# Performance work log

Hardware: AMD Instinct MI355X
Metric: run time of the kernel (lower is better)

## Reference

```python
import jax, jax.numpy as jnp
import numpy as np

THRESHOLD = 0.5
NEG_POS_RATIO = 3
ALPHA = 1.0


def xywh2xyxy(b):
    return jnp.concatenate([b[:, :2], b[:, :2] + b[:, 2:]], axis=1)


def cxcy2xyxy(b):
    return jnp.concatenate([b[:, :2] - b[:, 2:] / 2, b[:, :2] + b[:, 2:] / 2], axis=1)


def xyxy2cxcy(b):
    return jnp.concatenate([(b[:, :2] + b[:, 2:]) / 2, b[:, 2:] - b[:, :2]], axis=1)


def jaccard(a, b):
    # a: [n,4], b: [m,4] in xyxy -> IoU [n,m]
    lt = jnp.maximum(a[:, None, :2], b[None, :, :2])
    rb = jnp.minimum(a[:, None, 2:], b[None, :, 2:])
    wh = jnp.clip(rb - lt, 0.0)
    inter = wh[..., 0] * wh[..., 1]
    area_a = (a[:, 2] - a[:, 0]) * (a[:, 3] - a[:, 1])
    area_b = (b[:, 2] - b[:, 0]) * (b[:, 3] - b[:, 1])
    return inter / (area_a[:, None] + area_b[None, :] - inter)


def encode(cxcy, priors_cxcy):
    # cxcy_to_gcxgcy: offsets scaled by /10 variance, log sizes scaled by *5
    return jnp.concatenate([
        (cxcy[:, :2] - priors_cxcy[:, :2]) / (priors_cxcy[:, 2:] / 10.0),
        jnp.log(jnp.abs(cxcy[:, 2:] / priors_cxcy[:, 2:])) * 5.0,
    ], axis=1)


def _match_one(boxes_xywh, labels_i, priors_xy, priors_cxcy):
    n_obj = boxes_xywh.shape[0]
    b_xyxy = xywh2xyxy(boxes_xywh)                      # [n_obj,4]
    ov = jaccard(b_xyxy, priors_xy)                     # [n_obj, P]
    ovl_p = ov.max(axis=0)                              # [P]
    obj_p = ov.argmax(axis=0)                           # [P]
    prior_for_obj = ov.argmax(axis=1)                   # [n_obj]
    # force each object to own its best prior
    obj_p = obj_p.at[prior_for_obj].set(jnp.arange(n_obj))
    ovl_p = ovl_p.at[prior_for_obj].set(1.0)
    lab = labels_i[obj_p]                               # [P]
    lab = jnp.where(ovl_p < THRESHOLD, 0, lab)
    ignore = (ovl_p > 0.4) & (ovl_p < 0.5)
    true_locs = encode(xyxy2cxcy(b_xyxy[obj_p]), priors_cxcy)  # [P,4]
    return lab, ignore, true_locs


def _smooth_l1(x):
    ax = jnp.abs(x)
    return jnp.where(ax < 1.0, 0.5 * ax * ax, ax - 0.5)


def multibox_loss(predicted_locs, predicted_scores, boxes, labels, priors_cxcy):
    priors_xy = cxcy2xyxy(priors_cxcy)
    true_classes, ignored, true_locs = jax.vmap(
        _match_one, in_axes=(0, 0, None, None))(boxes, labels, priors_xy, priors_cxcy)
    pos = (true_classes > 0) & (~ignored)               # [B,P]
    n_pos = pos.sum(axis=1)                             # [B]
    n_pos_total = n_pos.sum()

    # localization loss: SmoothL1 mean over positive-prior elements
    loc_elem = _smooth_l1(predicted_locs - true_locs)   # [B,P,4]
    loc_loss = (loc_elem * pos[..., None]).sum() / (n_pos_total.astype(jnp.float32) * 4.0)

    # per-prior cross entropy
    logp = jax.nn.log_softmax(predicted_scores, axis=-1)           # [B,P,C]
    ce = -jnp.take_along_axis(logp, true_classes[..., None], axis=-1)[..., 0]  # [B,P]

    conf_pos_sum = (ce * pos).sum()
    ce_neg = jnp.where(pos | ignored, 0.0, ce)
    ce_neg_sorted = -jnp.sort(-ce_neg, axis=1)          # descending per row
    ranks = jnp.arange(ce.shape[1])[None, :]
    hard = ranks < (NEG_POS_RATIO * n_pos)[:, None]
    conf_loss = (jnp.where(hard, ce_neg_sorted, 0.0).sum() + conf_pos_sum) / n_pos_total.astype(jnp.float32)

    total = conf_loss + ALPHA * loc_loss
    return total, conf_loss, loc_loss


def setup_inputs() -> dict:
    key = jax.random.key(0)
    k1, k2, k3, k4, k5, k6 = jax.random.split(key, 6)
    B, P, C, NOBJ = 64, 8732, 91, 16
    predicted_locs = jax.random.normal(k1, (B, P, 4), dtype=jnp.float32)
    predicted_scores = jax.random.normal(k2, (B, P, C), dtype=jnp.float32)
    xy = jax.random.uniform(k3, (B, NOBJ, 2)) * 0.6
    wh = jax.random.uniform(k4, (B, NOBJ, 2)) * 0.35 + 0.05
    boxes = jnp.concatenate([xy, wh], axis=-1).astype(jnp.float32)  # xywh
    labels = jax.random.randint(k5, (B, NOBJ), 1, C)
    pxy = jax.random.uniform(k6, (P, 2))
    pwh = jax.random.uniform(jax.random.fold_in(k6, 1), (P, 2)) * 0.45 + 0.05
    priors_cxcy = jnp.concatenate([pxy, pwh], axis=-1).astype(jnp.float32)
    return {"predicted_locs": predicted_locs, "predicted_scores": predicted_scores,
            "boxes": boxes, "labels": labels, "priors_cxcy": priors_cxcy}


def reference(predicted_locs, predicted_scores, boxes, labels, priors_cxcy):
    return multibox_loss(predicted_locs, predicted_scores, boxes, labels, priors_cxcy)
```

## Files before the change

kernel.cpp:

```cpp
#include <hip/hip_runtime.h>
#include <math.h>

#define TPB 256
#define MTPB 512
#define CE_BLOCKS 2048

__device__ __forceinline__ float sl1(float x) {
    float a = fabsf(x);
    return a < 1.f ? 0.5f * a * a : a - 0.5f;
}

template<int NOBJ>
__global__ __launch_bounds__(MTPB)
void k_match(const float* __restrict__ boxes, const int* __restrict__ labels,
             const float* __restrict__ priors, const float* __restrict__ plocs,
             int P, unsigned* __restrict__ meta, int* __restrict__ n_pos,
             float* __restrict__ loc_sum, unsigned* __restrict__ ticket)
{
    const int b = blockIdx.x;
    const int tid = threadIdx.x;
    const int NW = MTPB / 64;

    if (b == 0 && tid == 0) *ticket = 0u;

    extern __shared__ char smem[];
    float* ovl_s = (float*)smem;
    unsigned char* obj_s = (unsigned char*)(smem + (size_t)P * 4);
    char* base2 = smem + (size_t)P * 4 + (size_t)((P + 15) & ~15);
    float* sbox2 = (float*)base2;
    int*   s_lab = (int*)(base2 + 4 * NOBJ * 4);
    float* redv  = (float*)(base2 + 5 * NOBJ * 4);
    int*   redp  = (int*)(base2 + (5 + NW) * NOBJ * 4);
    int*   pf    = (int*)(base2 + (5 + 2 * NW) * NOBJ * 4);
    int*   s_cnt = pf + NOBJ;
    float* s_lsum = (float*)(s_cnt + 1);

    float bx1[NOBJ], by1[NOBJ], bx2[NOBJ], by2[NOBJ], bar[NOBJ];
#pragma unroll
    for (int o = 0; o < NOBJ; o++) {
        const float4 bx = ((const float4*)boxes)[(size_t)b * NOBJ + o];
        bx1[o] = bx.x; by1[o] = bx.y;
        bx2[o] = bx.x + bx.z; by2[o] = bx.y + bx.w;
        bar[o] = (bx2[o] - bx1[o]) * (by2[o] - by1[o]);
    }
    if (tid < NOBJ) {
        sbox2[0 * NOBJ + tid] = (bx1[tid] + bx2[tid]) * 0.5f;
        sbox2[1 * NOBJ + tid] = (by1[tid] + by2[tid]) * 0.5f;
        sbox2[2 * NOBJ + tid] = bx2[tid] - bx1[tid];
        sbox2[3 * NOBJ + tid] = by2[tid] - by1[tid];
        s_lab[tid] = labels[b * NOBJ + tid];
        if (tid == 0) { *s_cnt = 0; *s_lsum = 0.f; }
    }

    float bestv[NOBJ];
    int bestp[NOBJ];
#pragma unroll
    for (int o = 0; o < NOBJ; o++) { bestv[o] = -1.f; bestp[o] = 0x7fffffff; }

    for (int p = tid; p < P; p += MTPB) {
        float4 pr = ((const float4*)priors)[p];
        float hx = pr.z * 0.5f, hy = pr.w * 0.5f;
        float px1 = pr.x - hx, py1 = pr.y - hy;
        float px2 = pr.x + hx, py2 = pr.y + hy;
        float parea = (px2 - px1) * (py2 - py1);
        float bv = -1.f; int bo = 0;
#pragma unroll
        for (int o = 0; o < NOBJ; o++) {
            float ltx = fmaxf(bx1[o], px1);
            float lty = fmaxf(by1[o], py1);
            float rbx = fminf(bx2[o], px2);
            float rby = fminf(by2[o], py2);
            float w = rbx - ltx; w = w > 0.f ? w : 0.f;
            float h = rby - lty; h = h > 0.f ? h : 0.f;
            float inter = w * h;
            float iou = __fdividef(inter, bar[o] + parea - inter);
            if (iou > bv) { bv = iou; bo = o; }
            if (iou > bestv[o]) { bestv[o] = iou; bestp[o] = p; }
        }
        ovl_s[p] = bv;
        obj_s[p] = (unsigned char)bo;
    }

#pragma unroll
    for (int o = 0; o < NOBJ; o++) {
        float v = bestv[o]; int pp = bestp[o];
#pragma unroll
        for (int d = 1; d < 64; d <<= 1) {
            float v2 = __shfl_xor(v, d);
            int   q2 = __shfl_xor(pp, d);
            if (v2 > v || (v2 == v && q2 < pp)) { v = v2; pp = q2; }
        }
        if ((tid & 63) == 0) {
            redv[o * NW + (tid >> 6)] = v;
            redp[o * NW + (tid >> 6)] = pp;
        }
    }
    __syncthreads();

    if (tid < NOBJ) {
        float v = -2.f; int pp = 0x7fffffff;
        for (int w = 0; w < NW; w++) {
            float v2 = redv[tid * NW + w];
            int   q2 = redp[tid * NW + w];
            if (v2 > v || (v2 == v && q2 < pp)) { v = v2; pp = q2; }
        }
        pf[tid] = pp;
    }
    __syncthreads();

    if (tid == 0) {
        for (int i = 0; i < NOBJ; i++) {
            int pp = pf[i];
            obj_s[pp] = (unsigned char)i;
            ovl_s[pp] = 1.0f;
        }
    }
    __syncthreads();

    int cnt = 0;
    float lsum = 0.f;
    for (int p = tid; p < P; p += MTPB) {
        float ovl = ovl_s[p];
        int o = obj_s[p];
        int lab = s_lab[o];
        if (ovl < 0.5f) lab = 0;
        bool ign = (ovl > 0.4f) && (ovl < 0.5f);
        bool pos = (lab > 0) && !ign;
        meta[(size_t)b * P + p] = (unsigned)lab | (pos ? 256u : 0u) | (ign ? 512u : 0u);
        if (pos) {
            cnt++;
            float4 pr = ((const float4*)priors)[p];
            float cx = sbox2[0 * NOBJ + o], cy = sbox2[1 * NOBJ + o];
            float bw = sbox2[2 * NOBJ + o], bh = sbox2[3 * NOBJ + o];
            float g0 = (cx - pr.x) / (pr.z / 10.0f);
            float g1 = (cy - pr.y) / (pr.w / 10.0f);
            float g2 = __logf(fabsf(bw / pr.z)) * 5.0f;
            float g3 = __logf(fabsf(bh / pr.w)) * 5.0f;
            float4 pl = ((const float4*)plocs)[(size_t)b * P + p];
            lsum += sl1(pl.x - g0) + sl1(pl.y - g1) + sl1(pl.z - g2) + sl1(pl.w - g3);
        }
    }
#pragma unroll
    for (int d = 1; d < 64; d <<= 1) {
        lsum += __shfl_xor(lsum, d);
        cnt  += __shfl_xor(cnt, d);
    }
    if ((tid & 63) == 0) {
        atomicAdd(s_cnt, cnt);
        atomicAdd(s_lsum, lsum);
    }
    __syncthreads();
    if (tid == 0) {
        n_pos[b] = *s_cnt;
        loc_sum[b] = *s_lsum;
    }
}

__global__ __launch_bounds__(TPB)
void k_ce(const float* __restrict__ scores, const unsigned* __restrict__ meta,
          int BP, int C, float* __restrict__ ce_neg, float* __restrict__ pos_blk)
{
    const int tid = threadIdx.x;
    const int g = tid >> 4;
    const int wg = (tid >> 4) & 3;
    const int l = tid & 15;
    const int tiles = BP >> 4;

    float psum = 0.f;

    for (int t = blockIdx.x; t < tiles; t += gridDim.x) {
        const int row = (t << 4) + g;
        const unsigned mt = meta[row];
        const float* s = scores + (size_t)row * C;

        float v[6];
        float m = -INFINITY;
#pragma unroll
        for (int j = 0; j < 6; j++) {
            int idx = l + (j << 4);
            v[j] = (idx < C) ? s[idx] : -INFINITY;
            m = fmaxf(m, v[j]);
        }
#pragma unroll
        for (int d = 1; d < 16; d <<= 1) m = fmaxf(m, __shfl_xor(m, d));

        float se = 0.f;
#pragma unroll
        for (int j = 0; j < 6; j++) se += __expf(v[j] - m);
#pragma unroll
        for (int d = 1; d < 16; d <<= 1) se += __shfl_xor(se, d);

        const int lab = (int)(mt & 255u);
        float pick = v[0];
#pragma unroll
        for (int j = 1; j < 6; j++) pick = ((lab >> 4) == j) ? v[j] : pick;
        float sv = __shfl(pick, (wg << 4) | (lab & 15));

        if (l == 0) {
            float ce = __logf(se) + m - sv;
            bool pos = (mt >> 8) & 1u;
            bool ign = (mt >> 9) & 1u;
            ce_neg[row] = (pos || ign) ? 0.f : ce;
            if (pos) psum += ce;
        }
    }

#pragma unroll
    for (int d = 1; d < 64; d <<= 1) psum += __shfl_xor(psum, d);
    __shared__ float sp[4];
    if ((tid & 63) == 0) sp[tid >> 6] = psum;
    __syncthreads();
    if (tid == 0) pos_blk[blockIdx.x] = sp[0] + sp[1] + sp[2] + sp[3];
}

template<int ITEMS>
__global__ __launch_bounds__(MTPB)
void k_topk_final(const float* __restrict__ ce_neg, const int* __restrict__ n_pos,
                  const float* __restrict__ loc_sum, const float* __restrict__ pos_blk,
                  int nposblk, int P, int B,
                  float* __restrict__ hard, unsigned* __restrict__ ticket,
                  float* __restrict__ out)
{
    const int b = blockIdx.x;
    const int tid = threadIdx.x;
    const float* row = ce_neg + (size_t)b * P;
    __shared__ unsigned cnt[256];
    __shared__ float sm[256];
    __shared__ float s_sumhigh;
    __shared__ unsigned s_pref;
    __shared__ int s_krem;
    __shared__ bool s_last;

    int k = 3 * n_pos[b];
    if (k > P) k = P;

    float vals[ITEMS];
#pragma unroll
    for (int i = 0; i < ITEMS; i++) {
        int p = tid + i * MTPB;
        vals[i] = (p < P) ? row[p] : 0.f;
    }

    float hard_b = 0.f;
    if (k > 0) {
        if (tid == 0) { s_sumhigh = 0.f; s_pref = 0u; s_krem = k; }

        for (int shift = 24; shift >= 0; shift -= 8) {
            if (tid < 256) { cnt[tid] = 0u; sm[tid] = 0.f; }
            __syncthreads();

            if (shift == 24) {
#pragma unroll
                for (int i = 0; i < ITEMS; i++) {
                    int p = tid + i * MTPB;
                    float vv = vals[i];
                    unsigned bin = __float_as_uint(vv) >> 24;
                    bool done = (p >= P);
                    while (__any(!done)) {
                        unsigned long long act = __ballot(!done);
                        int leader = (int)__ffsll(act) - 1;
                        unsigned lb = (unsigned)__shfl((int)bin, leader);
                        bool mine = (!done) && (bin == lb);
                        float contrib = mine ? vv : 0.f;
#pragma unroll
                        for (int d = 1; d < 64; d <<= 1)
                            contrib += __shfl_xor(contrib, d);
                        unsigned long long grp = __ballot(mine);
                        if ((tid & 63) == leader) {
                            atomicAdd(&cnt[lb], (unsigned)__popcll(grp));
                            atomicAdd(&sm[lb], contrib);
                        }
                        done = done || mine;
                    }
                }
            } else {
                unsigned pref = s_pref;
                const int high = shift + 8;
#pragma unroll
                for (int i = 0; i < ITEMS; i++) {
                    int p = tid + i * MTPB;
                    float vv = vals[i];
                    unsigned u = __float_as_uint(vv);
                    if (p < P && ((u >> high) == (pref >> high))) {
                        unsigned bin = (u >> shift) & 255u;
                        atomicAdd(&cnt[bin], 1u);
                        atomicAdd(&sm[bin], vv);
                    }
                }
            }
            __syncthreads();
            if (tid == 0) {
                int krem = s_krem;
                float sh = s_sumhigh;
                unsigned p2 = s_pref;
                for (int bin = 255; bin >= 0; --bin) {
                    if ((int)cnt[bin] < krem) { krem -= (int)cnt[bin]; sh += sm[bin]; }
                    else { p2 |= ((unsigned)bin) << shift; break; }
                }
                s_krem = krem; s_sumhigh = sh; s_pref = p2;
            }
            __syncthreads();
        }
        if (tid == 0) {
            float t = __uint_as_float(s_pref);
            hard_b = s_sumhigh + (float)s_krem * t;
        }
    }

    if (tid == 0) {
        atomicExch(&hard[b], hard_b);
        __threadfence();
        unsigned old = atomicAdd(ticket, 1u);
        s_last = (old == (unsigned)(gridDim.x - 1));
    }
    __syncthreads();
    if (!s_last) return;

    __threadfence();
    float hd = (tid < B) ? atomicAdd(&hard[tid], 0.f) : 0.f;
    float lc = (tid < B) ? loc_sum[tid] : 0.f;
    int   np = (tid < B) ? n_pos[tid] : 0;
    float ps = 0.f;
    for (int i = tid; i < nposblk; i += MTPB) ps += pos_blk[i];

#pragma unroll
    for (int d = 1; d < 64; d <<= 1) {
        hd += __shfl_xor(hd, d);
        lc += __shfl_xor(lc, d);
        ps += __shfl_xor(ps, d);
        np += __shfl_xor(np, d);
    }
    if ((tid & 63) == 0) {
        int wv = tid >> 6;
        sm[wv] = hd; sm[8 + wv] = lc; sm[16 + wv] = ps;
        cnt[wv] = (unsigned)np;
    }
    __syncthreads();
    if (tid == 0) {
        float thd = 0.f, tlc = 0.f, tps = 0.f; unsigned tnp = 0u;
        for (int wv = 0; wv < MTPB / 64; wv++) {
            thd += sm[wv]; tlc += sm[8 + wv]; tps += sm[16 + wv]; tnp += cnt[wv];
        }
        float n = (float)tnp;
        float conf = (thd + tps) / n;
        float loc = tlc / (n * 4.0f);
        out[0] = conf + loc;
        out[1] = conf;
        out[2] = loc;
    }
}

extern "C" void kernel_launch(void* const* d_in, const int* in_sizes, int n_in,
                              void* d_out, int out_size, void* d_ws, size_t ws_size,
                              hipStream_t stream)
{
    const float* plocs  = (const float*)d_in[0];
    const float* scores = (const float*)d_in[1];
    const float* boxes  = (const float*)d_in[2];
    const int*   labels = (const int*)d_in[3];
    const float* priors = (const float*)d_in[4];

    const int P = in_sizes[4] / 4;
    const int B = in_sizes[0] / (P * 4);
    const int C = in_sizes[1] / (B * P);
    const int BP = B * P;

    char* ws = (char*)d_ws;
    float*    loc_sum = (float*)ws;
    int*      n_pos   = (int*)(ws + 1024);
    float*    hard    = (float*)(ws + 2048);
    unsigned* ticket  = (unsigned*)(ws + 3072);
    unsigned* meta    = (unsigned*)(ws + 4096);
    float*    ce_neg  = (float*)(ws + 4096 + (size_t)BP * 4);
    float*    pos_blk = (float*)(ws + 4096 + (size_t)BP * 8);

    size_t ldsA = (size_t)P * 4 + (size_t)((P + 15) & ~15) + 2048;
    k_match<16><<<B, MTPB, ldsA, stream>>>(boxes, labels, priors, plocs,
                                           P, meta, n_pos, loc_sum, ticket);

    k_ce<<<CE_BLOCKS, TPB, 0, stream>>>(scores, meta, BP, C, ce_neg, pos_blk);

    if (P <= MTPB * 18) {
        k_topk_final<18><<<B, MTPB, 0, stream>>>(ce_neg, n_pos, loc_sum, pos_blk,
                                                 CE_BLOCKS, P, B, hard, ticket,
                                                 (float*)d_out);
    } else {
        k_topk_final<36><<<B, MTPB, 0, stream>>>(ce_neg, n_pos, loc_sum, pos_blk,
                                                 CE_BLOCKS, P, B, hard, ticket,
                                                 (float*)d_out);
    }
}
```

Measured before the change: 162.7 us.

## Split prior matching into segmented kernels and add vectorized C=91 CE kernel

The single per-image matching kernel, which ran only B blocks, is split into an IoU kernel and a finalize kernel. Each runs B*4 blocks over segments of priors and exchanges per-prior overlap and object index through global memory. Per-segment best-prior reductions are merged in the finalize step, and positive counts and loc sums are kept per segment. A specialized cross-entropy kernel for 91 classes loads four rows per wave as coalesced float4 reads staged through LDS. The aim is more GPU occupancy for matching and better memory efficiency for the score read, at the cost of an extra launch and a global round-trip for the overlap data.

```diff
diff --git a/kernel.cpp b/kernel.cpp
--- a/kernel.cpp
+++ b/kernel.cpp
@@ -4,6 +4,7 @@
 #define TPB 256
 #define MTPB 512
 #define CE_BLOCKS 2048
+#define SEGS 4
 
 __device__ __forceinline__ float sl1(float x) {
     float a = fabsf(x);
@@ -12,28 +13,25 @@
 
 template<int NOBJ>
 __global__ __launch_bounds__(MTPB)
-void k_match(const float* __restrict__ boxes, const int* __restrict__ labels,
-             const float* __restrict__ priors, const float* __restrict__ plocs,
-             int P, unsigned* __restrict__ meta, int* __restrict__ n_pos,
-             float* __restrict__ loc_sum, unsigned* __restrict__ ticket)
+void k_match_iou(const float* __restrict__ boxes, const float* __restrict__ priors,
+                 int P, float* __restrict__ ovl_g, unsigned char* __restrict__ obj_g,
+                 float* __restrict__ segv, int* __restrict__ segp,
+                 unsigned* __restrict__ ticket)
 {
-    const int b = blockIdx.x;
+    const int bs = blockIdx.x;
+    const int b = bs >> 2;
+    const int s = bs & 3;
     const int tid = threadIdx.x;
     const int NW = MTPB / 64;
 
-    if (b == 0 && tid == 0) *ticket = 0u;
-
-    extern __shared__ char smem[];
-    float* ovl_s = (float*)smem;
-    unsigned char* obj_s = (unsigned char*)(smem + (size_t)P * 4);
-    char* base2 = smem + (size_t)P * 4 + (size_t)((P + 15) & ~15);
-    float* sbox2 = (float*)base2;
-    int*   s_lab = (int*)(base2 + 4 * NOBJ * 4);
-    float* redv  = (float*)(base2 + 5 * NOBJ * 4);
-    int*   redp  = (int*)(base2 + (5 + NW) * NOBJ * 4);
-    int*   pf    = (int*)(base2 + (5 + 2 * NW) * NOBJ * 4);
-    int*   s_cnt = pf + NOBJ;
-    float* s_lsum = (float*)(s_cnt + 1);
+    if (bs == 0 && tid == 0) *ticket = 0u;
+
+    __shared__ float redv[NOBJ * (MTPB / 64)];
+    __shared__ int   redp[NOBJ * (MTPB / 64)];
+
+    const int seglen = (P + SEGS - 1) / SEGS;
+    const int p0 = s * seglen;
+    const int p1 = min(p0 + seglen, P);
 
     float bx1[NOBJ], by1[NOBJ], bx2[NOBJ], by2[NOBJ], bar[NOBJ];
 #pragma unroll
@@ -43,21 +41,13 @@
         bx2[o] = bx.x + bx.z; by2[o] = bx.y + bx.w;
         bar[o] = (bx2[o] - bx1[o]) * (by2[o] - by1[o]);
     }
-    if (tid < NOBJ) {
-        sbox2[0 * NOBJ + tid] = (bx1[tid] + bx2[tid]) * 0.5f;
-        sbox2[1 * NOBJ + tid] = (by1[tid] + by2[tid]) * 0.5f;
-        sbox2[2 * NOBJ + tid] = bx2[tid] - bx1[tid];
-        sbox2[3 * NOBJ + tid] = by2[tid] - by1[tid];
-        s_lab[tid] = labels[b * NOBJ + tid];
-        if (tid == 0) { *s_cnt = 0; *s_lsum = 0.f; }
-    }
 
     float bestv[NOBJ];
     int bestp[NOBJ];
 #pragma unroll
     for (int o = 0; o < NOBJ; o++) { bestv[o] = -1.f; bestp[o] = 0x7fffffff; }
 
-    for (int p = tid; p < P; p += MTPB) {
+    for (int p = p0 + tid; p < p1; p += MTPB) {
         float4 pr = ((const float4*)priors)[p];
         float hx = pr.z * 0.5f, hy = pr.w * 0.5f;
         float px1 = pr.x - hx, py1 = pr.y - hy;
@@ -77,8 +67,8 @@
             if (iou > bv) { bv = iou; bo = o; }
             if (iou > bestv[o]) { bestv[o] = iou; bestp[o] = p; }
         }
-        ovl_s[p] = bv;
-        obj_s[p] = (unsigned char)bo;
+        ovl_g[(size_t)b * P + p] = bv;
+        obj_g[(size_t)b * P + p] = (unsigned char)bo;
     }
 
 #pragma unroll
@@ -104,24 +94,65 @@
             int   q2 = redp[tid * NW + w];
             if (v2 > v || (v2 == v && q2 < pp)) { v = v2; pp = q2; }
         }
+        segv[((size_t)b * NOBJ + tid) * SEGS + s] = v;
+        segp[((size_t)b * NOBJ + tid) * SEGS + s] = pp;
+    }
+}
+
+template<int NOBJ>
+__global__ __launch_bounds__(MTPB)
+void k_match_fin(const float* __restrict__ boxes, const int* __restrict__ labels,
+                 const float* __restrict__ priors, const float* __restrict__ plocs,
+                 const float* __restrict__ ovl_g, const unsigned char* __restrict__ obj_g,
+                 const float* __restrict__ segv, const int* __restrict__ segp,
+                 int P, unsigned* __restrict__ meta,
+                 int* __restrict__ n_pos_seg, float* __restrict__ loc_seg)
+{
+    const int bs = blockIdx.x;
+    const int b = bs >> 2;
+    const int s = bs & 3;
+    const int tid = threadIdx.x;
+
+    __shared__ float sbox2[4 * NOBJ];
+    __shared__ int s_lab[NOBJ];
+    __shared__ int pf[NOBJ];
+    __shared__ int s_cnt;
+    __shared__ float s_lsum;
+
+    if (tid < NOBJ) {
+        const float4 bx = ((const float4*)boxes)[(size_t)b * NOBJ + tid];
+        float x1 = bx.x, y1 = bx.y, x2 = bx.x + bx.z, y2 = bx.y + bx.w;
+        sbox2[0 * NOBJ + tid] = (x1 + x2) * 0.5f;
+        sbox2[1 * NOBJ + tid] = (y1 + y2) * 0.5f;
+        sbox2[2 * NOBJ + tid] = x2 - x1;
+        sbox2[3 * NOBJ + tid] = y2 - y1;
+        s_lab[tid] = labels[b * NOBJ + tid];
+        float v = -2.f; int pp = 0x7fffffff;
+#pragma unroll
+        for (int ss = 0; ss < SEGS; ss++) {
+            float v2 = segv[((size_t)b * NOBJ + tid) * SEGS + ss];
+            int   q2 = segp[((size_t)b * NOBJ + tid) * SEGS + ss];
+            if (v2 > v || (v2 == v && q2 < pp)) { v = v2; pp = q2; }
+        }
         pf[tid] = pp;
-    }
-    __syncthreads();
-
-    if (tid == 0) {
-        for (int i = 0; i < NOBJ; i++) {
-            int pp = pf[i];
-            obj_s[pp] = (unsigned char)i;
-            ovl_s[pp] = 1.0f;
-        }
-    }
-    __syncthreads();
+        if (tid == 0) { s_cnt = 0; s_lsum = 0.f; }
+    }
+    __syncthreads();
+
+    const int seglen = (P + SEGS - 1) / SEGS;
+    const int p0 = s * seglen;
+    const int p1 = min(p0 + seglen, P);
 
     int cnt = 0;
     float lsum = 0.f;
-    for (int p = tid; p < P; p += MTPB) {
-        float ovl = ovl_s[p];
-        int o = obj_s[p];
+    for (int p = p0 + tid; p < p1; p += MTPB) {
+        float ovl = ovl_g[(size_t)b * P + p];
+        int o = obj_g[(size_t)b * P + p];
+        int fo = -1;
+#pragma unroll
+        for (int i = 0; i < NOBJ; i++) if (pf[i] == p) fo = i;
+        if (fo >= 0) { ovl = 1.0f; o = fo; }
+
         int lab = s_lab[o];
         if (ovl < 0.5f) lab = 0;
         bool ign = (ovl > 0.4f) && (ovl < 0.5f);
@@ -146,14 +177,80 @@
         cnt  += __shfl_xor(cnt, d);
     }
     if ((tid & 63) == 0) {
-        atomicAdd(s_cnt, cnt);
-        atomicAdd(s_lsum, lsum);
+        atomicAdd(&s_cnt, cnt);
+        atomicAdd(&s_lsum, lsum);
     }
     __syncthreads();
     if (tid == 0) {
-        n_pos[b] = *s_cnt;
-        loc_sum[b] = *s_lsum;
-    }
+        n_pos_seg[bs] = s_cnt;
+        loc_seg[bs] = s_lsum;
+    }
+}
+
+__global__ __launch_bounds__(TPB)
+void k_ce91(const float* __restrict__ scores, const unsigned* __restrict__ meta,
+            int BP, float* __restrict__ ce_neg, float* __restrict__ pos_blk)
+{
+    __shared__ __align__(16) float sf[4 * 364];
+    __shared__ float sp[4];
+
+    const int tid = threadIdx.x;
+    const int wid = tid >> 6;
+    const int lane = tid & 63;
+    const int g = (tid >> 4) & 3;
+    const int l = tid & 15;
+    float* wlds = sf + wid * 364;
+
+    const int nquads = BP >> 2;
+    const int gwaves = gridDim.x * (TPB / 64);
+    const float4* src = (const float4*)scores;
+
+    float psum = 0.f;
+
+    for (int q = blockIdx.x * (TPB / 64) + wid; q < nquads; q += gwaves) {
+        float4 ra = src[(size_t)q * 91 + lane];
+        float4 rb = make_float4(0.f, 0.f, 0.f, 0.f);
+        if (lane < 27) rb = src[(size_t)q * 91 + 64 + lane];
+        unsigned mt = 0u;
+        if (l == 0) mt = meta[(q << 2) + g];
+
+        ((float4*)wlds)[lane] = ra;
+        if (lane < 27) ((float4*)wlds)[64 + lane] = rb;
+
+        const float* rowp = wlds + g * 91;
+        float v[6];
+        float m = -INFINITY;
+#pragma unroll
+        for (int j = 0; j < 6; j++) {
+            int idx = l + (j << 4);
+            v[j] = (idx < 91) ? rowp[idx] : -INFINITY;
+            m = fmaxf(m, v[j]);
+        }
+#pragma unroll
+        for (int d = 1; d < 16; d <<= 1) m = fmaxf(m, __shfl_xor(m, d));
+
+        float se = 0.f;
+#pragma unroll
+        for (int j = 0; j < 6; j++) se += __expf(v[j] - m);
+#pragma unroll
+        for (int d = 1; d < 16; d <<= 1) se += __shfl_xor(se, d);
+
+        if (l == 0) {
+            int lab = (int)(mt & 255u);
+            float sv = rowp[lab];
+            float ce = __logf(se) + m - sv;
+            bool pos = (mt >> 8) & 1u;
+            bool ign = (mt >> 9) & 1u;
+            ce_neg[(q << 2) + g] = (pos || ign) ? 0.f : ce;
+            if (pos) psum += ce;
+        }
+    }
+
+#pragma unroll
+    for (int d = 1; d < 64; d <<= 1) psum += __shfl_xor(psum, d);
+    if ((tid & 63) == 0) sp[tid >> 6] = psum;
+    __syncthreads();
+    if (tid == 0) pos_blk[blockIdx.x] = sp[0] + sp[1] + sp[2] + sp[3];
 }
 
 __global__ __launch_bounds__(TPB)
@@ -215,8 +312,8 @@
 
 template<int ITEMS>
 __global__ __launch_bounds__(MTPB)
-void k_topk_final(const float* __restrict__ ce_neg, const int* __restrict__ n_pos,
-                  const float* __restrict__ loc_sum, const float* __restrict__ pos_blk,
+void k_topk_final(const float* __restrict__ ce_neg, const int* __restrict__ n_pos_seg,
+                  const float* __restrict__ loc_seg, const float* __restrict__ pos_blk,
                   int nposblk, int P, int B,
                   float* __restrict__ hard, unsigned* __restrict__ ticket,
                   float* __restrict__ out)
@@ -231,7 +328,10 @@
     __shared__ int s_krem;
     __shared__ bool s_last;
 
-    int k = 3 * n_pos[b];
+    int k = 0;
+#pragma unroll
+    for (int s = 0; s < SEGS; s++) k += n_pos_seg[b * SEGS + s];
+    k *= 3;
     if (k > P) k = P;
 
     float vals[ITEMS];
@@ -318,8 +418,11 @@
 
     __threadfence();
     float hd = (tid < B) ? atomicAdd(&hard[tid], 0.f) : 0.f;
-    float lc = (tid < B) ? loc_sum[tid] : 0.f;
-    int   np = (tid < B) ? n_pos[tid] : 0;
+    float lc = 0.f; int np = 0;
+    for (int i = tid; i < B * SEGS; i += MTPB) {
+        lc += loc_seg[i];
+        np += n_pos_seg[i];
+    }
     float ps = 0.f;
     for (int i = tid; i < nposblk; i += MTPB) ps += pos_blk[i];
 
@@ -364,28 +467,41 @@
     const int B = in_sizes[0] / (P * 4);
     const int C = in_sizes[1] / (B * P);
     const int BP = B * P;
+    const int NOBJ = 16;
 
     char* ws = (char*)d_ws;
-    float*    loc_sum = (float*)ws;
-    int*      n_pos   = (int*)(ws + 1024);
-    float*    hard    = (float*)(ws + 2048);
-    unsigned* ticket  = (unsigned*)(ws + 3072);
-    unsigned* meta    = (unsigned*)(ws + 4096);
-    float*    ce_neg  = (float*)(ws + 4096 + (size_t)BP * 4);
-    float*    pos_blk = (float*)(ws + 4096 + (size_t)BP * 8);
-
-    size_t ldsA = (size_t)P * 4 + (size_t)((P + 15) & ~15) + 2048;
-    k_match<16><<<B, MTPB, ldsA, stream>>>(boxes, labels, priors, plocs,
-                                           P, meta, n_pos, loc_sum, ticket);
-
-    k_ce<<<CE_BLOCKS, TPB, 0, stream>>>(scores, meta, BP, C, ce_neg, pos_blk);
+    float*    loc_seg   = (float*)ws;
+    int*      n_pos_seg = (int*)(ws + 1024);
+    float*    hard      = (float*)(ws + 2048);
+    unsigned* ticket    = (unsigned*)(ws + 3072);
+    unsigned* meta      = (unsigned*)(ws + 4096);
+    float*    ce_neg    = (float*)(ws + 4096 + (size_t)BP * 4);
+    float*    pos_blk   = (float*)(ws + 4096 + (size_t)BP * 8);
+    char*     ws2       = ws + 4096 + (size_t)BP * 8 + 8192;
+    float*    segv      = (float*)ws2;
+    int*      segp      = (int*)(ws2 + 16384);
+    float*    ovl_g     = (float*)(ws2 + 32768);
+    unsigned char* obj_g = (unsigned char*)(ws2 + 32768 + (size_t)BP * 4);
+
+    k_match_iou<16><<<B * SEGS, MTPB, 0, stream>>>(boxes, priors, P,
+                                                   ovl_g, obj_g, segv, segp, ticket);
+
+    k_match_fin<16><<<B * SEGS, MTPB, 0, stream>>>(boxes, labels, priors, plocs,
+                                                   ovl_g, obj_g, segv, segp,
+                                                   P, meta, n_pos_seg, loc_seg);
+
+    if (C == 91 && (BP & 3) == 0) {
+        k_ce91<<<CE_BLOCKS, TPB, 0, stream>>>(scores, meta, BP, ce_neg, pos_blk);
+    } else {
+        k_ce<<<CE_BLOCKS, TPB, 0, stream>>>(scores, meta, BP, C, ce_neg, pos_blk);
+    }
 
     if (P <= MTPB * 18) {
-        k_topk_final<18><<<B, MTPB, 0, stream>>>(ce_neg, n_pos, loc_sum, pos_blk,
+        k_topk_final<18><<<B, MTPB, 0, stream>>>(ce_neg, n_pos_seg, loc_seg, pos_blk,
                                                  CE_BLOCKS, P, B, hard, ticket,
                                                  (float*)d_out);
     } else {
-        k_topk_final<36><<<B, MTPB, 0, stream>>>(ce_neg, n_pos, loc_sum, pos_blk,
+        k_topk_final<36><<<B, MTPB, 0, stream>>>(ce_neg, n_pos_seg, loc_seg, pos_blk,
                                                  CE_BLOCKS, P, B, hard, ticket,
                                                  (float*)d_out);
     }
```

New measurement: 133.2 us. 1.22x faster.
